# Kernel tuning notes

Hardware: AMD Instinct MI355X
Metric: run time of the kernel (lower is better)

## Reference

```python
import jax, jax.numpy as jnp
import numpy as np

N_NODES = 100000
N_EDGES = 1600000
N_FEAT = 512
N_HID = 256
N_CLASS = 40


def setup_inputs() -> dict:
    key = jax.random.key(0)
    ks = jax.random.split(key, 6)
    features = jax.random.normal(ks[0], (N_NODES, N_FEAT), dtype=jnp.float32)
    edge_index = jax.random.randint(ks[1], (2, N_EDGES), 0, N_NODES, dtype=jnp.int32)
    edge_weight = jax.random.uniform(ks[2], (N_EDGES,), dtype=jnp.float32)
    # xavier_uniform with gain=1.414 (as in reset_parameters)
    g = 1.414
    lim1 = g * np.sqrt(6.0 / (N_FEAT + N_HID))
    lim2 = g * np.sqrt(6.0 / (N_HID + N_CLASS))
    W1 = jax.random.uniform(ks[3], (N_FEAT, N_HID), minval=-lim1, maxval=lim1, dtype=jnp.float32)
    W2 = jax.random.uniform(ks[4], (N_HID, N_CLASS), minval=-lim2, maxval=lim2, dtype=jnp.float32)
    b1 = jnp.zeros((N_HID,), dtype=jnp.float32)
    b2 = jnp.zeros((N_CLASS,), dtype=jnp.float32)
    return {"features": features, "edge_index": edge_index, "edge_weight": edge_weight,
            "W1": W1, "b1": b1, "W2": W2, "b2": b2}


def _spmm(edge_index, edge_weight, x, n):
    # out[r] = sum over edges e with row[e]==r of w[e] * x[col[e]]
    row, col = edge_index[0], edge_index[1]
    msgs = edge_weight[:, None] * x[col]  # [E, D]
    return jax.ops.segment_sum(msgs, row, num_segments=n)


def reference(features, edge_index, edge_weight, W1, b1, W2, b2):
    n = features.shape[0]
    # Layer 1: linear -> spmm -> relu (dropout is identity in eval mode)
    h = features @ W1 + b1
    h = jax.nn.relu(_spmm(edge_index, edge_weight, h, n))
    # Layer 2: linear -> spmm -> log_softmax
    h = h @ W2 + b2
    h = _spmm(edge_index, edge_weight, h, n)
    return jax.nn.log_softmax(h, axis=1)
```

## Files before the change

kernel.cpp:

```cpp
#include <hip/hip_runtime.h>
#include <stdint.h>

#define N_NODES 100000
#define N_EDGES 1600000
#define N_FEAT 512
#define N_HID 256
#define N_CLASS 40
#define H2SB 64

typedef float f32x4 __attribute__((ext_vector_type(4)));
typedef __bf16 bf16x8 __attribute__((ext_vector_type(8)));
typedef unsigned short u16x4 __attribute__((ext_vector_type(4)));
typedef unsigned short u16x8 __attribute__((ext_vector_type(8)));

__device__ __forceinline__ unsigned short f2bf(float f) {
  unsigned int u = __float_as_uint(f);
  unsigned int r = (u + 0x7FFFu + ((u >> 16) & 1u)) >> 16;
  return (unsigned short)r;
}
__device__ __forceinline__ float bf2f(unsigned short s) {
  return __uint_as_float(((unsigned int)s) << 16);
}
__device__ __forceinline__ float pk_w(unsigned int p) {
  return __uint_as_float((p >> 17) << 16);
}
__device__ __forceinline__ int pk_c(unsigned int p) { return (int)(p & 0x1FFFFu); }

__global__ __launch_bounds__(1024) void k_zero(int* __restrict__ cnt) {
  int i = blockIdx.x * 1024 + threadIdx.x;
  if (i < N_NODES) cnt[i] = 0;
}

#define HIST_BLOCKS 1563
#define W1T_BLOCKS  512
#define W2T_BLOCKS  48
__global__ __launch_bounds__(256) void k_pre(const float* __restrict__ W1,
                                             const float* __restrict__ W2,
                                             const int* __restrict__ ei,
                                             unsigned short* __restrict__ W1t,
                                             unsigned short* __restrict__ W2t,
                                             int* __restrict__ cnt,
                                             int* __restrict__ rank) {
  const int bid = blockIdx.x, tid = threadIdx.x;
  if (bid < HIST_BLOCKS) {
    #pragma unroll
    for (int k = 0; k < 4; ++k) {
      int e = bid * 1024 + k * 256 + tid;
      if (e < N_EDGES) rank[e] = atomicAdd(&cnt[ei[e]], 1);
    }
  } else if (bid < HIST_BLOCKS + W1T_BLOCKS) {
    int gid = (bid - HIST_BLOCKS) * 256 + tid;
    int n = gid >> 9, k = gid & 511;
    W1t[gid] = f2bf(W1[(long)k * N_HID + n]);
  } else {
    int gid = (bid - HIST_BLOCKS - W1T_BLOCKS) * 256 + tid;
    int n = gid >> 8, k = gid & 255;
    W2t[gid] = (n < N_CLASS) ? f2bf(W2[(long)k * N_CLASS + n]) : (unsigned short)0;
  }
}

__global__ __launch_bounds__(1024) void k_scan_a(const int* __restrict__ cnt,
                                                 int* __restrict__ rp,
                                                 int* __restrict__ bsum) {
  __shared__ int sm[1024];
  const int tid = threadIdx.x;
  const int i = blockIdx.x * 1024 + tid;
  int v = (i < N_NODES) ? cnt[i] : 0;
  sm[tid] = v;
  __syncthreads();
  #pragma unroll
  for (int d = 1; d < 1024; d <<= 1) {
    int t = (tid >= d) ? sm[tid - d] : 0;
    __syncthreads();
    sm[tid] += t;
    __syncthreads();
  }
  if (i < N_NODES) rp[i] = sm[tid] - v;
  if (tid == 1023) bsum[blockIdx.x] = sm[1023];
}

__global__ __launch_bounds__(128) void k_scan_b(const int* __restrict__ bsum,
                                                int* __restrict__ boffs,
                                                int* __restrict__ rp) {
  __shared__ int sm[128];
  const int tid = threadIdx.x;
  const int nb = (N_NODES + 1023) >> 10;
  int v = (tid < nb) ? bsum[tid] : 0;
  sm[tid] = v;
  __syncthreads();
  #pragma unroll
  for (int d = 1; d < 128; d <<= 1) {
    int t = (tid >= d) ? sm[tid - d] : 0;
    __syncthreads();
    sm[tid] += t;
    __syncthreads();
  }
  boffs[tid] = sm[tid] - v;
  if (tid == 127) rp[N_NODES] = sm[127];
}

__global__ void k_scan_c(int* __restrict__ rp, const int* __restrict__ boffs) {
  int i = blockIdx.x * 256 + threadIdx.x;
  if (i >= N_NODES) return;
  rp[i] += boffs[i >> 10];
}

#define G1_BLOCKS 391
__global__ __launch_bounds__(1024) void k_gemm1(const float* __restrict__ X,
                                                const unsigned short* __restrict__ W1t,
                                                const float* __restrict__ b1,
                                                unsigned short* __restrict__ H1,
                                                const int* __restrict__ ei,
                                                const float* __restrict__ ew,
                                                const int* __restrict__ rank,
                                                const int* __restrict__ rp,
                                                unsigned int* __restrict__ cwp) {
  __shared__ __align__(16) unsigned short Bs[256 * 256];
  const int t = threadIdx.x;
  const long rb = (long)blockIdx.x * 256;
  const int lane = t & 63;
  const int wid = t >> 6;
  const int lr = lane & 15;
  const int lkg = lane >> 4;

  long myrow = rb + wid * 16 + lr;
  if (myrow >= N_NODES) myrow = N_NODES - 1;
  const float* xrow = X + myrow * N_FEAT;

  f32x4 acc[16] = {};

  #pragma unroll 1
  for (int kc = 0; kc < 2; ++kc) {
    __syncthreads();
    {
      const int col = t >> 2;
      const int sg = (t & 3) * 8;
      const unsigned short* src = W1t + (long)col * N_FEAT + kc * 256;
      #pragma unroll
      for (int j = 0; j < 8; ++j) {
        int slot = sg + j;
        int ps = slot ^ (col & 7);
        *(u16x8*)&Bs[col * 256 + ps * 8] = *(const u16x8*)(src + slot * 8);
      }
    }
    __syncthreads();

    bf16x8 av[8];
    #pragma unroll
    for (int ks = 0; ks < 8; ++ks) {
      const float* xp = xrow + kc * 256 + ks * 32 + lkg * 8;
      f32x4 xa = __builtin_nontemporal_load((const f32x4*)xp);
      f32x4 xb = __builtin_nontemporal_load((const f32x4*)(xp + 4));
      bf16x8 v;
      v[0] = (__bf16)xa[0]; v[1] = (__bf16)xa[1];
      v[2] = (__bf16)xa[2]; v[3] = (__bf16)xa[3];
      v[4] = (__bf16)xb[0]; v[5] = (__bf16)xb[1];
      v[6] = (__bf16)xb[2]; v[7] = (__bf16)xb[3];
      av[ks] = v;
    }

    #pragma unroll
    for (int ks = 0; ks < 8; ++ks) {
      const int slot = ks * 4 + lkg;
      const int ps = slot ^ (lr & 7);
      #pragma unroll
      for (int nt = 0; nt < 16; ++nt) {
        bf16x8 bv = *(const bf16x8*)&Bs[(nt * 16 + lr) * 256 + ps * 8];
        acc[nt] = __builtin_amdgcn_mfma_f32_16x16x32_bf16(av[ks], bv, acc[nt], 0, 0, 0);
      }
    }
  }

  #pragma unroll
  for (int nt = 0; nt < 16; ++nt) {
    int colg = nt * 16 + lr;
    float bias = b1[colg];
    #pragma unroll
    for (int i = 0; i < 4; ++i) {
      long row = rb + wid * 16 + lkg * 4 + i;
      if (row < N_NODES) H1[row * N_HID + colg] = f2bf(acc[nt][i] + bias);
    }
  }

  #pragma unroll
  for (int k = 0; k < 4; ++k) {
    int e = blockIdx.x * 4096 + k * 1024 + t;
    if (e < N_EDGES) {
      int r = ei[e];
      int pos = rp[r] + rank[e];
      unsigned int w15 = (unsigned int)f2bf(ew[e]);
      cwp[pos] = (w15 << 17) | (unsigned int)ei[N_EDGES + e];
    }
  }
}

__global__ __launch_bounds__(256) void k_spmm1(const int* __restrict__ row_ptr,
                                               const unsigned int* __restrict__ cwp,
                                               const unsigned short* __restrict__ H1,
                                               unsigned short* __restrict__ H1r) {
  int r = blockIdx.x * 8 + (threadIdx.x >> 5);
  int lane = threadIdx.x & 31;
  if (r >= N_NODES) return;
  int s = row_ptr[r], e = row_ptr[r + 1];
  float a0 = 0.f, a1 = 0.f, a2 = 0.f, a3 = 0.f;
  float a4 = 0.f, a5 = 0.f, a6 = 0.f, a7 = 0.f;
  const unsigned short* Hb = H1 + lane * 8;
  int i = s;
  uint4 q0 = {}, q1 = {};
  if (i + 8 <= e) { q0 = *(const uint4*)(cwp + i); q1 = *(const uint4*)(cwp + i + 4); }
  for (; i + 8 <= e; ) {
    unsigned int cc[8] = {q0.x, q0.y, q0.z, q0.w, q1.x, q1.y, q1.z, q1.w};
    const int inext = i + 8;
    if (inext + 8 <= e) {
      q0 = *(const uint4*)(cwp + inext);
      q1 = *(const uint4*)(cwp + inext + 4);
    }
    u16x8 h[8];
    #pragma unroll
    for (int j = 0; j < 8; ++j)
      h[j] = *(const u16x8*)(Hb + (long)pk_c(cc[j]) * N_HID);
    #pragma unroll
    for (int j = 0; j < 8; ++j) {
      float w = pk_w(cc[j]);
      a0 += w * bf2f(h[j][0]);
      a1 += w * bf2f(h[j][1]);
      a2 += w * bf2f(h[j][2]);
      a3 += w * bf2f(h[j][3]);
      a4 += w * bf2f(h[j][4]);
      a5 += w * bf2f(h[j][5]);
      a6 += w * bf2f(h[j][6]);
      a7 += w * bf2f(h[j][7]);
    }
    i = inext;
  }
  for (; i < e; ++i) {
    unsigned int p = cwp[i];
    float w = pk_w(p);
    u16x8 hv = *(const u16x8*)(Hb + (long)pk_c(p) * N_HID);
    a0 += w * bf2f(hv[0]);
    a1 += w * bf2f(hv[1]);
    a2 += w * bf2f(hv[2]);
    a3 += w * bf2f(hv[3]);
    a4 += w * bf2f(hv[4]);
    a5 += w * bf2f(hv[5]);
    a6 += w * bf2f(hv[6]);
    a7 += w * bf2f(hv[7]);
  }
  u16x8 o;
  o[0] = f2bf(fmaxf(a0, 0.f));
  o[1] = f2bf(fmaxf(a1, 0.f));
  o[2] = f2bf(fmaxf(a2, 0.f));
  o[3] = f2bf(fmaxf(a3, 0.f));
  o[4] = f2bf(fmaxf(a4, 0.f));
  o[5] = f2bf(fmaxf(a5, 0.f));
  o[6] = f2bf(fmaxf(a6, 0.f));
  o[7] = f2bf(fmaxf(a7, 0.f));
  *(u16x8*)(H1r + (long)r * N_HID + lane * 8) = o;
}

__global__ __launch_bounds__(256) void k_gemm2(const unsigned short* __restrict__ H1r,
                                               const unsigned short* __restrict__ W2t,
                                               const float* __restrict__ b2,
                                               unsigned short* __restrict__ H2) {
  const int t = threadIdx.x;
  const int lane = t & 63;
  const int wid = t >> 6;
  const long m0 = (long)blockIdx.x * 128;
  const int lr = lane & 15;
  const int lk = (lane >> 4) * 8;

  const unsigned short* Ab[2];
  #pragma unroll
  for (int mt = 0; mt < 2; ++mt) {
    long r = m0 + wid * 32 + mt * 16 + lr;
    if (r >= N_NODES) r = N_NODES - 1;
    Ab[mt] = H1r + r * N_HID + lk;
  }
  const unsigned short* Bb[3];
  #pragma unroll
  for (int nt = 0; nt < 3; ++nt)
    Bb[nt] = W2t + (long)(nt * 16 + lr) * N_HID + lk;

  f32x4 acc[2][3] = {};
  #pragma unroll
  for (int k0 = 0; k0 < N_HID; k0 += 32) {
    bf16x8 av[2], bvv[3];
    #pragma unroll
    for (int mt = 0; mt < 2; ++mt) av[mt] = *(const bf16x8*)(Ab[mt] + k0);
    #pragma unroll
    for (int nt = 0; nt < 3; ++nt) bvv[nt] = *(const bf16x8*)(Bb[nt] + k0);
    #pragma unroll
    for (int mt = 0; mt < 2; ++mt)
      #pragma unroll
      for (int nt = 0; nt < 3; ++nt)
        acc[mt][nt] = __builtin_amdgcn_mfma_f32_16x16x32_bf16(av[mt], bvv[nt], acc[mt][nt], 0, 0, 0);
  }

  #pragma unroll
  for (int nt = 0; nt < 3; ++nt) {
    int col = nt * 16 + lr;
    if (col < N_CLASS) {
      float bias = b2[col];
      #pragma unroll
      for (int mt = 0; mt < 2; ++mt) {
        #pragma unroll
        for (int i = 0; i < 4; ++i) {
          long row = m0 + wid * 32 + mt * 16 + (lane >> 4) * 4 + i;
          if (row < N_NODES) H2[row * H2SB + col] = f2bf(acc[mt][nt][i] + bias);
        }
      }
    }
  }
}

__global__ __launch_bounds__(256) void k_spmm2_lsm(const int* __restrict__ row_ptr,
                                                   const unsigned int* __restrict__ cwp,
                                                   const unsigned short* __restrict__ H2,
                                                   float* __restrict__ out) {
  int r = blockIdx.x * 4 + (threadIdx.x >> 6);
  int lane = threadIdx.x & 63;
  if (r >= N_NODES) return;
  int s = row_ptr[r], e = row_ptr[r + 1];
  float acc = 0.f;
  const bool act = lane < N_CLASS;
  int i = s;
  for (; i + 8 <= e; i += 8) {
    uint4 q0 = *(const uint4*)(cwp + i);
    uint4 q1 = *(const uint4*)(cwp + i + 4);
    unsigned int cc[8] = {q0.x, q0.y, q0.z, q0.w, q1.x, q1.y, q1.z, q1.w};
    float h[8];
    #pragma unroll
    for (int j = 0; j < 8; ++j)
      h[j] = act ? bf2f(H2[(long)pk_c(cc[j]) * H2SB + lane]) : 0.f;
    #pragma unroll
    for (int j = 0; j < 8; ++j) acc += pk_w(cc[j]) * h[j];
  }
  for (; i < e; ++i) {
    unsigned int p = cwp[i];
    if (act) acc += pk_w(p) * bf2f(H2[(long)pk_c(p) * H2SB + lane]);
  }
  float v = act ? acc : -INFINITY;
  float m = v;
  #pragma unroll
  for (int d = 32; d > 0; d >>= 1) m = fmaxf(m, __shfl_xor(m, d));
  float ex = act ? __expf(v - m) : 0.f;
  float ssum = ex;
  #pragma unroll
  for (int d = 32; d > 0; d >>= 1) ssum += __shfl_xor(ssum, d);
  float ls = __logf(ssum);
  if (act) out[(long)r * N_CLASS + lane] = v - m - ls;
}

extern "C" void kernel_launch(void* const* d_in, const int* in_sizes, int n_in,
                              void* d_out, int out_size, void* d_ws, size_t ws_size,
                              hipStream_t stream) {
  (void)in_sizes; (void)n_in; (void)out_size; (void)ws_size;
  const float* X  = (const float*)d_in[0];
  const int*   EI = (const int*)d_in[1];
  const float* EW = (const float*)d_in[2];
  const float* W1 = (const float*)d_in[3];
  const float* b1 = (const float*)d_in[4];
  const float* W2 = (const float*)d_in[5];
  const float* b2 = (const float*)d_in[6];
  float* out = (float*)d_out;

  char* p = (char*)d_ws;
  auto take = [&](size_t bytes) {
    char* r = p;
    p += (bytes + 511) & ~(size_t)511;
    return r;
  };
  unsigned short* W1t   = (unsigned short*)take((size_t)N_HID * N_FEAT * 2);
  unsigned short* W2t   = (unsigned short*)take((size_t)48 * N_HID * 2);
  int*            cnt   = (int*)take((size_t)N_NODES * 4);
  int*            rp    = (int*)take((size_t)(N_NODES + 1) * 4);
  int*            bsum  = (int*)take((size_t)128 * 4);
  int*            boffs = (int*)take((size_t)128 * 4);
  int*            rank  = (int*)take((size_t)N_EDGES * 4);
  unsigned int*   cwp   = (unsigned int*)take((size_t)N_EDGES * 4);
  unsigned short* H1    = (unsigned short*)take((size_t)N_NODES * N_HID * 2);
  unsigned short* H1r   = (unsigned short*)take((size_t)N_NODES * N_HID * 2);
  unsigned short* H2    = (unsigned short*)take((size_t)N_NODES * H2SB * 2);

  const int NB_SCAN = (N_NODES + 1023) / 1024;

  k_zero<<<NB_SCAN, 1024, 0, stream>>>(cnt);
  k_pre<<<HIST_BLOCKS + W1T_BLOCKS + W2T_BLOCKS, 256, 0, stream>>>(W1, W2, EI, W1t, W2t, cnt, rank);
  k_scan_a<<<NB_SCAN, 1024, 0, stream>>>(cnt, rp, bsum);
  k_scan_b<<<1, 128, 0, stream>>>(bsum, boffs, rp);
  k_scan_c<<<(N_NODES + 255) / 256, 256, 0, stream>>>(rp, boffs);
  k_gemm1<<<G1_BLOCKS, 1024, 0, stream>>>(X, W1t, b1, H1, EI, EW, rank, rp, cwp);
  k_spmm1<<<(N_NODES + 7) / 8, 256, 0, stream>>>(rp, cwp, H1, H1r);
  k_gemm2<<<(N_NODES + 127) / 128, 256, 0, stream>>>(H1r, W2t, b2, H2);
  k_spmm2_lsm<<<(N_NODES + 3) / 4, 256, 0, stream>>>(rp, cwp, H2, out);
}
```

Before: 447.3 us.

## Fuse spmm1 with gemm2, split edge scatter out of gemm1, prefetch X

Folds the second linear layer into the first SpMM kernel: each row's ReLU output is staged in shared memory and multiplied by W2 with scalar dot products. This removes the H1r intermediate round trip and the separate gemm2 launch. The CSR edge scatter moves out of gemm1 into its own kernel, and gemm1 now loads the second K-chunk of X early so the load overlaps the MFMA work. The costs are gemm2 running on scalar FMAs instead of MFMA (about 48 column dots per row, with redundant W2 reads) and one extra kernel launch.

```diff
diff --git a/kernel.cpp b/kernel.cpp
--- a/kernel.cpp
+++ b/kernel.cpp
@@ -105,16 +105,29 @@
   rp[i] += boffs[i >> 10];
 }
 
+__global__ __launch_bounds__(512) void k_scatter(const int* __restrict__ ei,
+                                                 const float* __restrict__ ew,
+                                                 const int* __restrict__ rank,
+                                                 const int* __restrict__ rp,
+                                                 unsigned int* __restrict__ cwp) {
+  const int t = threadIdx.x;
+  #pragma unroll
+  for (int k = 0; k < 4; ++k) {
+    int e = blockIdx.x * 2048 + k * 512 + t;
+    if (e < N_EDGES) {
+      int r = ei[e];
+      int pos = rp[r] + rank[e];
+      unsigned int w15 = (unsigned int)f2bf(ew[e]);
+      cwp[pos] = (w15 << 17) | (unsigned int)ei[N_EDGES + e];
+    }
+  }
+}
+
 #define G1_BLOCKS 391
 __global__ __launch_bounds__(1024) void k_gemm1(const float* __restrict__ X,
                                                 const unsigned short* __restrict__ W1t,
                                                 const float* __restrict__ b1,
-                                                unsigned short* __restrict__ H1,
-                                                const int* __restrict__ ei,
-                                                const float* __restrict__ ew,
-                                                const int* __restrict__ rank,
-                                                const int* __restrict__ rp,
-                                                unsigned int* __restrict__ cwp) {
+                                                unsigned short* __restrict__ H1) {
   __shared__ __align__(16) unsigned short Bs[256 * 256];
   const int t = threadIdx.x;
   const long rb = (long)blockIdx.x * 256;
@@ -128,6 +141,14 @@
   const float* xrow = X + myrow * N_FEAT;
 
   f32x4 acc[16] = {};
+
+  f32x4 xa[8], xb[8];
+  #pragma unroll
+  for (int ks = 0; ks < 8; ++ks) {
+    const float* xp = xrow + ks * 32 + lkg * 8;
+    xa[ks] = __builtin_nontemporal_load((const f32x4*)xp);
+    xb[ks] = __builtin_nontemporal_load((const f32x4*)(xp + 4));
+  }
 
   #pragma unroll 1
   for (int kc = 0; kc < 2; ++kc) {
@@ -148,15 +169,21 @@
     bf16x8 av[8];
     #pragma unroll
     for (int ks = 0; ks < 8; ++ks) {
-      const float* xp = xrow + kc * 256 + ks * 32 + lkg * 8;
-      f32x4 xa = __builtin_nontemporal_load((const f32x4*)xp);
-      f32x4 xb = __builtin_nontemporal_load((const f32x4*)(xp + 4));
       bf16x8 v;
-      v[0] = (__bf16)xa[0]; v[1] = (__bf16)xa[1];
-      v[2] = (__bf16)xa[2]; v[3] = (__bf16)xa[3];
-      v[4] = (__bf16)xb[0]; v[5] = (__bf16)xb[1];
-      v[6] = (__bf16)xb[2]; v[7] = (__bf16)xb[3];
+      v[0] = (__bf16)xa[ks][0]; v[1] = (__bf16)xa[ks][1];
+      v[2] = (__bf16)xa[ks][2]; v[3] = (__bf16)xa[ks][3];
+      v[4] = (__bf16)xb[ks][0]; v[5] = (__bf16)xb[ks][1];
+      v[6] = (__bf16)xb[ks][2]; v[7] = (__bf16)xb[ks][3];
       av[ks] = v;
+    }
+
+    if (kc == 0) {
+      #pragma unroll
+      for (int ks = 0; ks < 8; ++ks) {
+        const float* xp = xrow + 256 + ks * 32 + lkg * 8;
+        xa[ks] = __builtin_nontemporal_load((const f32x4*)xp);
+        xb[ks] = __builtin_nontemporal_load((const f32x4*)(xp + 4));
+      }
     }
 
     #pragma unroll
@@ -181,26 +208,18 @@
       if (row < N_NODES) H1[row * N_HID + colg] = f2bf(acc[nt][i] + bias);
     }
   }
-
-  #pragma unroll
-  for (int k = 0; k < 4; ++k) {
-    int e = blockIdx.x * 4096 + k * 1024 + t;
-    if (e < N_EDGES) {
-      int r = ei[e];
-      int pos = rp[r] + rank[e];
-      unsigned int w15 = (unsigned int)f2bf(ew[e]);
-      cwp[pos] = (w15 << 17) | (unsigned int)ei[N_EDGES + e];
-    }
-  }
-}
-
-__global__ __launch_bounds__(256) void k_spmm1(const int* __restrict__ row_ptr,
-                                               const unsigned int* __restrict__ cwp,
-                                               const unsigned short* __restrict__ H1,
-                                               unsigned short* __restrict__ H1r) {
-  int r = blockIdx.x * 8 + (threadIdx.x >> 5);
-  int lane = threadIdx.x & 31;
-  if (r >= N_NODES) return;
+}
+
+__global__ __launch_bounds__(256) void k_spmm1f(const int* __restrict__ row_ptr,
+                                                const unsigned int* __restrict__ cwp,
+                                                const unsigned short* __restrict__ H1,
+                                                const unsigned short* __restrict__ W2t,
+                                                const float* __restrict__ b2,
+                                                unsigned short* __restrict__ H2) {
+  __shared__ unsigned short hs[8][256];
+  const int g = threadIdx.x >> 5;
+  const int lane = threadIdx.x & 31;
+  const int r = blockIdx.x * 8 + g;
   int s = row_ptr[r], e = row_ptr[r + 1];
   float a0 = 0.f, a1 = 0.f, a2 = 0.f, a3 = 0.f;
   float a4 = 0.f, a5 = 0.f, a6 = 0.f, a7 = 0.f;
@@ -255,62 +274,26 @@
   o[5] = f2bf(fmaxf(a5, 0.f));
   o[6] = f2bf(fmaxf(a6, 0.f));
   o[7] = f2bf(fmaxf(a7, 0.f));
-  *(u16x8*)(H1r + (long)r * N_HID + lane * 8) = o;
-}
-
-__global__ __launch_bounds__(256) void k_gemm2(const unsigned short* __restrict__ H1r,
-                                               const unsigned short* __restrict__ W2t,
-                                               const float* __restrict__ b2,
-                                               unsigned short* __restrict__ H2) {
-  const int t = threadIdx.x;
-  const int lane = t & 63;
-  const int wid = t >> 6;
-  const long m0 = (long)blockIdx.x * 128;
-  const int lr = lane & 15;
-  const int lk = (lane >> 4) * 8;
-
-  const unsigned short* Ab[2];
-  #pragma unroll
-  for (int mt = 0; mt < 2; ++mt) {
-    long r = m0 + wid * 32 + mt * 16 + lr;
-    if (r >= N_NODES) r = N_NODES - 1;
-    Ab[mt] = H1r + r * N_HID + lk;
-  }
-  const unsigned short* Bb[3];
-  #pragma unroll
-  for (int nt = 0; nt < 3; ++nt)
-    Bb[nt] = W2t + (long)(nt * 16 + lr) * N_HID + lk;
-
-  f32x4 acc[2][3] = {};
-  #pragma unroll
-  for (int k0 = 0; k0 < N_HID; k0 += 32) {
-    bf16x8 av[2], bvv[3];
-    #pragma unroll
-    for (int mt = 0; mt < 2; ++mt) av[mt] = *(const bf16x8*)(Ab[mt] + k0);
-    #pragma unroll
-    for (int nt = 0; nt < 3; ++nt) bvv[nt] = *(const bf16x8*)(Bb[nt] + k0);
-    #pragma unroll
-    for (int mt = 0; mt < 2; ++mt)
-      #pragma unroll
-      for (int nt = 0; nt < 3; ++nt)
-        acc[mt][nt] = __builtin_amdgcn_mfma_f32_16x16x32_bf16(av[mt], bvv[nt], acc[mt][nt], 0, 0, 0);
-  }
-
-  #pragma unroll
-  for (int nt = 0; nt < 3; ++nt) {
-    int col = nt * 16 + lr;
-    if (col < N_CLASS) {
-      float bias = b2[col];
-      #pragma unroll
-      for (int mt = 0; mt < 2; ++mt) {
-        #pragma unroll
-        for (int i = 0; i < 4; ++i) {
-          long row = m0 + wid * 32 + mt * 16 + (lane >> 4) * 4 + i;
-          if (row < N_NODES) H2[row * H2SB + col] = f2bf(acc[mt][nt][i] + bias);
-        }
-      }
-    }
-  }
+  *(u16x8*)&hs[g][lane * 8] = o;
+  __syncthreads();
+
+  const int c2 = (lane + 32 < 48) ? lane + 32 : 47;
+  float acc1 = 0.f, acc2 = 0.f;
+  const unsigned short* w1p = W2t + (long)lane * N_HID;
+  const unsigned short* w2p = W2t + (long)c2 * N_HID;
+  #pragma unroll 4
+  for (int k0 = 0; k0 < N_HID; k0 += 8) {
+    bf16x8 hv = *(const bf16x8*)&hs[g][k0];
+    bf16x8 w1 = *(const bf16x8*)(w1p + k0);
+    bf16x8 w2 = *(const bf16x8*)(w2p + k0);
+    #pragma unroll
+    for (int j = 0; j < 8; ++j) {
+      acc1 += (float)hv[j] * (float)w1[j];
+      acc2 += (float)hv[j] * (float)w2[j];
+    }
+  }
+  H2[(long)r * H2SB + lane] = f2bf(acc1 + b2[lane]);
+  if (lane < N_CLASS - 32) H2[(long)r * H2SB + 32 + lane] = f2bf(acc2 + b2[32 + lane]);
 }
 
 __global__ __launch_bounds__(256) void k_spmm2_lsm(const int* __restrict__ row_ptr,
@@ -379,7 +362,6 @@
   int*            rank  = (int*)take((size_t)N_EDGES * 4);
   unsigned int*   cwp   = (unsigned int*)take((size_t)N_EDGES * 4);
   unsigned short* H1    = (unsigned short*)take((size_t)N_NODES * N_HID * 2);
-  unsigned short* H1r   = (unsigned short*)take((size_t)N_NODES * N_HID * 2);
   unsigned short* H2    = (unsigned short*)take((size_t)N_NODES * H2SB * 2);
 
   const int NB_SCAN = (N_NODES + 1023) / 1024;
@@ -389,8 +371,8 @@
   k_scan_a<<<NB_SCAN, 1024, 0, stream>>>(cnt, rp, bsum);
   k_scan_b<<<1, 128, 0, stream>>>(bsum, boffs, rp);
   k_scan_c<<<(N_NODES + 255) / 256, 256, 0, stream>>>(rp, boffs);
-  k_gemm1<<<G1_BLOCKS, 1024, 0, stream>>>(X, W1t, b1, H1, EI, EW, rank, rp, cwp);
-  k_spmm1<<<(N_NODES + 7) / 8, 256, 0, stream>>>(rp, cwp, H1, H1r);
-  k_gemm2<<<(N_NODES + 127) / 128, 256, 0, stream>>>(H1r, W2t, b2, H2);
+  k_scatter<<<(N_EDGES + 2047) / 2048, 512, 0, stream>>>(EI, EW, rank, rp, cwp);
+  k_gemm1<<<G1_BLOCKS, 1024, 0, stream>>>(X, W1t, b1, H1);
+  k_spmm1f<<<N_NODES / 8, 256, 0, stream>>>(rp, cwp, H1, W2t, b2, H2);
   k_spmm2_lsm<<<(N_NODES + 3) / 4, 256, 0, stream>>>(rp, cwp, H2, out);
 }
```

Result: slower. 811.7 us (+81.5%).
